# Performance work log

Hardware: AMD Instinct MI355X
Metric: run time of the kernel (lower is better)

The kernel has to match this reference:

```python
import jax, jax.numpy as jnp
import numpy as np

NUM_QUBITS = 11
STATE_SIZE = 2 ** NUM_QUBITS  # 2048
FUSION_DIM = 2048
THETA = np.pi / 4


def _apply_hadamards(state):
    # state: [B, 2**n] complex. Apply H to every qubit (qubit q <-> bit 2**q,
    # matching the original's little-endian index arithmetic).
    B, S = state.shape
    inv_sqrt2 = jnp.asarray(1.0 / np.sqrt(2.0), dtype=state.dtype)
    for q in range(NUM_QUBITS):
        # index = hi * 2**(q+1) + b * 2**q + lo
        s = state.reshape(B, S >> (q + 1), 2, 1 << q)
        a, b = s[:, :, 0, :], s[:, :, 1, :]
        s = jnp.stack([(a + b) * inv_sqrt2, (a - b) * inv_sqrt2], axis=2)
        state = s.reshape(B, S)
    return state


def _rz_diag():
    # RZ(theta) on every qubit is diagonal: phase exp(+i*theta/2) if bit set,
    # exp(-i*theta/2) otherwise -> total phase depends only on popcount.
    idx = jnp.arange(STATE_SIZE)
    bits = (idx[:, None] >> jnp.arange(NUM_QUBITS)[None, :]) & 1  # [S, n]
    popcount = bits.sum(axis=-1).astype(jnp.float32)
    phase = (THETA / 2.0) * (2.0 * popcount - NUM_QUBITS)
    return jnp.exp(1j * phase).astype(jnp.complex64)  # [S]


def setup_inputs() -> dict:
    key = jax.random.key(0)
    k1, k2 = jax.random.split(key)
    x1 = jax.random.normal(k1, (8192, 1024), dtype=jnp.float32)
    x2 = jax.random.normal(k2, (8192, 1024), dtype=jnp.float32)
    return {"x1": x1, "x2": x2}


def reference(x1, x2):
    combined = jnp.concatenate([x1, x2], axis=-1)  # [B, D]
    B, D = combined.shape
    m = min(D, STATE_SIZE)
    # _prepare_quantum_state: embed first min(D, 2**n) features as complex amplitudes
    state = jnp.zeros((B, STATE_SIZE), dtype=jnp.complex64)
    state = state.at[:, :m].set(combined[:, :m].astype(jnp.complex64))
    # H on every qubit
    state = _apply_hadamards(state)
    # CNOT chain: the original swaps each (i, i^target) pair twice -> identity.
    # Faithfully reproduced as a no-op.
    # RZ on every qubit (diagonal phase)
    state = state * _rz_diag()[None, :]
    # _measure_quantum_state: probabilities, then pad/truncate to fusion_dim
    feats = (jnp.abs(state) ** 2).astype(jnp.float32)  # [B, 2**n]
    if feats.shape[1] < FUSION_DIM:
        feats = jnp.pad(feats, ((0, 0), (0, FUSION_DIM - feats.shape[1])))
    elif feats.shape[1] > FUSION_DIM:
        feats = feats[:, :FUSION_DIM]
    return feats
```

## Files before the change

kernel.cpp:

```cpp
#include <hip/hip_runtime.h>


template <int CTRL>
__device__ __forceinline__ float dpp_xmov(float x) {
    return __int_as_float(__builtin_amdgcn_update_dpp(
        0, __float_as_int(x), CTRL, 0xF, 0xF, true));
}

__global__ __launch_bounds__(256) void qf_wht_kernel(const float* __restrict__ x1,
                                                     const float* __restrict__ x2,
                                                     float* __restrict__ out,
                                                     int nrows) {
    const int wave = threadIdx.x >> 6;
    const int lane = threadIdx.x & 63;
    const int row  = blockIdx.x * 4 + wave;
    if (row >= nrows) return;

    float v[32];

    const float* __restrict__ p1 = x1 + (size_t)row * 1024 + lane * 4;
    const float* __restrict__ p2 = x2 + (size_t)row * 1024 + lane * 4;
#pragma unroll
    for (int jo = 0; jo < 4; ++jo) {
        float4 f = *(const float4*)(p1 + jo * 256);
        v[jo * 4 + 0] = f.x; v[jo * 4 + 1] = f.y;
        v[jo * 4 + 2] = f.z; v[jo * 4 + 3] = f.w;
    }
#pragma unroll
    for (int jo = 4; jo < 8; ++jo) {
        float4 f = *(const float4*)(p2 + (jo - 4) * 256);
        v[jo * 4 + 0] = f.x; v[jo * 4 + 1] = f.y;
        v[jo * 4 + 2] = f.z; v[jo * 4 + 3] = f.w;
    }

#pragma unroll
    for (int m = 1; m < 32; m <<= 1) {
#pragma unroll
        for (int j = 0; j < 32; ++j) {
            if ((j & m) == 0) {
                const float a = v[j];
                const float b = v[j | m];
                v[j]     = a + b;
                v[j | m] = a - b;
            }
        }
    }

    {
        const float s = (lane & 1) ? -1.0f : 1.0f;
#pragma unroll
        for (int j = 0; j < 32; ++j) {
            const float p = dpp_xmov<0xB1>(v[j]);
            v[j] = fmaf(s, v[j], p);
        }
    }
    {
        const float s = (lane & 2) ? -1.0f : 1.0f;
#pragma unroll
        for (int j = 0; j < 32; ++j) {
            const float p = dpp_xmov<0x4E>(v[j]);
            v[j] = fmaf(s, v[j], p);
        }
    }
    {
        const float s = (lane & 4) ? -1.0f : 1.0f;
#pragma unroll
        for (int j = 0; j < 32; ++j) {
            const float p = dpp_xmov<0x141>(dpp_xmov<0x1B>(v[j]));
            v[j] = fmaf(s, v[j], p);
        }
    }
    {
        const float s = (lane & 8) ? -1.0f : 1.0f;
#pragma unroll
        for (int j = 0; j < 32; ++j) {
            const float p = dpp_xmov<0x140>(dpp_xmov<0x141>(v[j]));
            v[j] = fmaf(s, v[j], p);
        }
    }
    {
        const float s = (lane & 16) ? -1.0f : 1.0f;
#pragma unroll
        for (int j = 0; j < 32; ++j) {
            const float p = __int_as_float(
                __builtin_amdgcn_ds_swizzle(__float_as_int(v[j]), 0x401F));
            v[j] = fmaf(s, v[j], p);
        }
    }
    {
        const float s = (lane & 32) ? -1.0f : 1.0f;
        const int idx32 = (lane ^ 32) << 2;
#pragma unroll
        for (int j = 0; j < 32; ++j) {
            const float p = __int_as_float(
                __builtin_amdgcn_ds_bpermute(idx32, __float_as_int(v[j])));
            v[j] = fmaf(s, v[j], p);
        }
    }

    const float scale = 1.0f / 2048.0f;
    float* __restrict__ po = out + (size_t)row * 2048 + lane * 4;
#pragma unroll
    for (int jo = 0; jo < 8; ++jo) {
        float4 f;
        f.x = v[jo * 4 + 0] * v[jo * 4 + 0] * scale;
        f.y = v[jo * 4 + 1] * v[jo * 4 + 1] * scale;
        f.z = v[jo * 4 + 2] * v[jo * 4 + 2] * scale;
        f.w = v[jo * 4 + 3] * v[jo * 4 + 3] * scale;
        *(float4*)(po + jo * 256) = f;
    }
}

extern "C" void kernel_launch(void* const* d_in, const int* in_sizes, int n_in,
                              void* d_out, int out_size, void* d_ws, size_t ws_size,
                              hipStream_t stream) {
    const float* x1 = (const float*)d_in[0];
    const float* x2 = (const float*)d_in[1];
    float* out = (float*)d_out;

    const int nrows = in_sizes[0] / 1024;
    const int blocks = (nrows + 3) / 4;
    qf_wht_kernel<<<blocks, 256, 0, stream>>>(x1, x2, out, nrows);
}
```

Baseline: 111.7 us.

## Process two rows per wave with 64 registers per lane, dropping the bpermute stage

Each wave now handles two rows, 32 lanes per row, with 64 values per lane. That moves one more butterfly stage into registers and removes the cross-half ds_bpermute stage, which went through LDS hardware. The scale is applied before squaring to keep magnitudes stable. The cost is doubled register use per thread, which lowers occupancy for a kernel that is mostly bound by memory bandwidth.

```diff
diff --git a/kernel.cpp b/kernel.cpp
--- a/kernel.cpp
+++ b/kernel.cpp
@@ -13,30 +13,32 @@
                                                      int nrows) {
     const int wave = threadIdx.x >> 6;
     const int lane = threadIdx.x & 63;
-    const int row  = blockIdx.x * 4 + wave;
+    const int half = lane >> 5;
+    const int l5   = lane & 31;
+    const int row  = blockIdx.x * 8 + wave * 2 + half;
     if (row >= nrows) return;
 
-    float v[32];
+    float v[64];
 
-    const float* __restrict__ p1 = x1 + (size_t)row * 1024 + lane * 4;
-    const float* __restrict__ p2 = x2 + (size_t)row * 1024 + lane * 4;
+    const float* __restrict__ p1 = x1 + (size_t)row * 1024 + l5 * 4;
+    const float* __restrict__ p2 = x2 + (size_t)row * 1024 + l5 * 4;
 #pragma unroll
-    for (int jo = 0; jo < 4; ++jo) {
-        float4 f = *(const float4*)(p1 + jo * 256);
-        v[jo * 4 + 0] = f.x; v[jo * 4 + 1] = f.y;
-        v[jo * 4 + 2] = f.z; v[jo * 4 + 3] = f.w;
+    for (int ro = 0; ro < 8; ++ro) {
+        float4 f = *(const float4*)(p1 + ro * 128);
+        v[ro * 4 + 0] = f.x; v[ro * 4 + 1] = f.y;
+        v[ro * 4 + 2] = f.z; v[ro * 4 + 3] = f.w;
     }
 #pragma unroll
-    for (int jo = 4; jo < 8; ++jo) {
-        float4 f = *(const float4*)(p2 + (jo - 4) * 256);
-        v[jo * 4 + 0] = f.x; v[jo * 4 + 1] = f.y;
-        v[jo * 4 + 2] = f.z; v[jo * 4 + 3] = f.w;
+    for (int ro = 8; ro < 16; ++ro) {
+        float4 f = *(const float4*)(p2 + (ro - 8) * 128);
+        v[ro * 4 + 0] = f.x; v[ro * 4 + 1] = f.y;
+        v[ro * 4 + 2] = f.z; v[ro * 4 + 3] = f.w;
     }
 
 #pragma unroll
-    for (int m = 1; m < 32; m <<= 1) {
+    for (int m = 1; m < 64; m <<= 1) {
 #pragma unroll
-        for (int j = 0; j < 32; ++j) {
+        for (int j = 0; j < 64; ++j) {
             if ((j & m) == 0) {
                 const float a = v[j];
                 const float b = v[j | m];
@@ -49,7 +51,7 @@
     {
         const float s = (lane & 1) ? -1.0f : 1.0f;
 #pragma unroll
-        for (int j = 0; j < 32; ++j) {
+        for (int j = 0; j < 64; ++j) {
             const float p = dpp_xmov<0xB1>(v[j]);
             v[j] = fmaf(s, v[j], p);
         }
@@ -57,7 +59,7 @@
     {
         const float s = (lane & 2) ? -1.0f : 1.0f;
 #pragma unroll
-        for (int j = 0; j < 32; ++j) {
+        for (int j = 0; j < 64; ++j) {
             const float p = dpp_xmov<0x4E>(v[j]);
             v[j] = fmaf(s, v[j], p);
         }
@@ -65,7 +67,7 @@
     {
         const float s = (lane & 4) ? -1.0f : 1.0f;
 #pragma unroll
-        for (int j = 0; j < 32; ++j) {
+        for (int j = 0; j < 64; ++j) {
             const float p = dpp_xmov<0x141>(dpp_xmov<0x1B>(v[j]));
             v[j] = fmaf(s, v[j], p);
         }
@@ -73,7 +75,7 @@
     {
         const float s = (lane & 8) ? -1.0f : 1.0f;
 #pragma unroll
-        for (int j = 0; j < 32; ++j) {
+        for (int j = 0; j < 64; ++j) {
             const float p = dpp_xmov<0x140>(dpp_xmov<0x141>(v[j]));
             v[j] = fmaf(s, v[j], p);
         }
@@ -81,33 +83,22 @@
     {
         const float s = (lane & 16) ? -1.0f : 1.0f;
 #pragma unroll
-        for (int j = 0; j < 32; ++j) {
+        for (int j = 0; j < 64; ++j) {
             const float p = __int_as_float(
                 __builtin_amdgcn_ds_swizzle(__float_as_int(v[j]), 0x401F));
             v[j] = fmaf(s, v[j], p);
         }
     }
-    {
-        const float s = (lane & 32) ? -1.0f : 1.0f;
-        const int idx32 = (lane ^ 32) << 2;
+
+    const float c = 0.022097086912079608f;
+    float* __restrict__ po = out + (size_t)row * 2048 + l5 * 4;
 #pragma unroll
-        for (int j = 0; j < 32; ++j) {
-            const float p = __int_as_float(
-                __builtin_amdgcn_ds_bpermute(idx32, __float_as_int(v[j])));
-            v[j] = fmaf(s, v[j], p);
-        }
-    }
-
-    const float scale = 1.0f / 2048.0f;
-    float* __restrict__ po = out + (size_t)row * 2048 + lane * 4;
-#pragma unroll
-    for (int jo = 0; jo < 8; ++jo) {
+    for (int ro = 0; ro < 16; ++ro) {
         float4 f;
-        f.x = v[jo * 4 + 0] * v[jo * 4 + 0] * scale;
-        f.y = v[jo * 4 + 1] * v[jo * 4 + 1] * scale;
-        f.z = v[jo * 4 + 2] * v[jo * 4 + 2] * scale;
-        f.w = v[jo * 4 + 3] * v[jo * 4 + 3] * scale;
-        *(float4*)(po + jo * 256) = f;
+        float t0 = v[ro * 4 + 0] * c, t1 = v[ro * 4 + 1] * c;
+        float t2 = v[ro * 4 + 2] * c, t3 = v[ro * 4 + 3] * c;
+        f.x = t0 * t0; f.y = t1 * t1; f.z = t2 * t2; f.w = t3 * t3;
+        *(float4*)(po + ro * 128) = f;
     }
 }
 
@@ -119,6 +110,6 @@
     float* out = (float*)d_out;
 
     const int nrows = in_sizes[0] / 1024;
-    const int blocks = (nrows + 3) / 4;
+    const int blocks = (nrows + 7) / 8;
     qf_wht_kernel<<<blocks, 256, 0, stream>>>(x1, x2, out, nrows);
 }
```

Result: no change. 113.5 us (+1.7%).
